# Optimization experiments

Hardware: AMD Instinct MI355X
Metric: run time of the kernel (lower is better)

Reference implementation:

```python
import jax, jax.numpy as jnp
import numpy as np

S = 14       # grid size
B = 2        # boxes per cell
C = 20       # classes
N_EL = B * 5 + C   # 30
L_COORD = 5.0
L_NOOBJ = 0.5
BATCH = 4096
NBOX = 16


def setup_inputs() -> dict:
    key = jax.random.key(0)
    k1, k2, k3, k4 = jax.random.split(key, 4)
    prediction = jax.random.uniform(k1, (BATCH, S * S * N_EL), dtype=jnp.float32)
    # well-formed ground-truth boxes: centers in (0.05,0.95), sizes in (0.02,0.3)
    cxcy = jax.random.uniform(k2, (BATCH, NBOX, 2), minval=0.05, maxval=0.95, dtype=jnp.float32)
    wh = jax.random.uniform(k3, (BATCH, NBOX, 2), minval=0.02, maxval=0.3, dtype=jnp.float32)
    boxes = jnp.concatenate([cxcy - wh / 2, cxcy + wh / 2], axis=-1)  # x1,y1,x2,y2
    classes = jax.random.randint(k4, (BATCH, NBOX), 0, C, dtype=jnp.int32)
    return {"prediction": prediction, "boxes": boxes, "classes": classes}


def _encode(boxes, classes):
    """Vectorized version of YoloLoss.encode: scatter boxes into SxS grid cells.
    Faithful detail: class one-hot goes to channel 9+class (the original's
    off-by-one: class 0 lands on the 2nd confidence channel)."""
    bsz, nbox = classes.shape
    cell = 1.0 / S
    xy1, xy2 = boxes[..., :2], boxes[..., 2:]
    wh = xy2 - xy1
    cxcy = (xy1 + xy2) / 2
    ij = jnp.clip(jnp.ceil(cxcy / cell) - 1, 0, S - 1)          # [b,nbox,2] (x,y)
    dxy = cxcy / cell - ij                                      # delta inside cell
    ij = ij.astype(jnp.int32)
    one = jnp.ones_like(wh[..., :1])
    zcls = jnp.zeros(classes.shape + (C,), dtype=boxes.dtype)
    # layout: [dxy, wh, conf, dxy, wh, conf, class one-hots]
    base = jnp.concatenate([dxy, wh, one, dxy, wh, one, zcls], axis=-1)  # [b,nbox,30]
    cls_oh = jax.nn.one_hot(classes + (B * 5 - 1), N_EL, dtype=boxes.dtype)  # index 9+class
    vec = jnp.maximum(base, cls_oh)
    flat_idx = (jnp.arange(bsz, dtype=jnp.int32)[:, None] * (S * S)
                + ij[..., 1] * S + ij[..., 0]).reshape(-1)      # row-major (y,x)
    target = jnp.zeros((bsz * S * S, N_EL), dtype=boxes.dtype)
    return target.at[flat_idx].set(vec.reshape(-1, N_EL))


def _pairwise_iou(a, b):
    """a,b: [N,B,4] -> iou [N,B(pred),B(target)] (corner-format jaccard, as in
    the original, applied to (dx,dy,w,h) rows verbatim)."""
    a4 = a[:, :, None, :]
    b4 = b[:, None, :, :]
    lt = jnp.maximum(a4[..., :2], b4[..., :2])
    rb = jnp.minimum(a4[..., 2:], b4[..., 2:])
    whi = jnp.clip(rb - lt, 0.0)
    inter = whi[..., 0] * whi[..., 1]
    area_a = (a4[..., 2] - a4[..., 0]) * (a4[..., 3] - a4[..., 1])
    area_b = (b4[..., 2] - b4[..., 0]) * (b4[..., 3] - b4[..., 1])
    union = area_a + area_b - inter
    return inter / jnp.where(union == 0, 1.0, union)


def reference(prediction, boxes, classes):
    target = _encode(boxes, classes)                       # [bsz*S*S, 30]
    pred = prediction.reshape(-1, N_EL)
    coord = target[:, 4] > 0                               # cells containing objects
    coordf = coord.astype(pred.dtype)
    noobjf = (target[:, 4] == 0).astype(pred.dtype)

    conf_idx = jnp.array([4, 9])
    noobj_loss = jnp.sum(noobjf[:, None] * (pred[:, conf_idx] - target[:, conf_idx]) ** 2)
    class_loss = jnp.sum(coordf[:, None] * (pred[:, B * 5:] - target[:, B * 5:]) ** 2)

    bp = pred[:, :B * 5].reshape(-1, B, 5)                 # [N,B,5]
    bt = target[:, :B * 5].reshape(-1, B, 5)

    iou = _pairwise_iou(bp[..., :4], bt[..., :4])          # [N,B,B]
    max_index = jnp.argmax(iou, axis=1)                    # best pred per target box
    response = (max_index[:, None, :] == jnp.arange(B)[None, :, None]).any(-1)  # [N,B]
    resp = response & coord[:, None]
    respf = resp.astype(pred.dtype)

    contain_loss = jnp.sum(respf * (bp[..., 4] - bt[..., 4]) ** 2)
    bt_wh = jnp.where(resp[..., None], bt[..., 2:4], 1.0)  # guard sqrt at masked cells
    loc_loss = jnp.sum(respf * (((bp[..., :2] - bt[..., :2]) ** 2).sum(-1)
                                + ((jnp.sqrt(bp[..., 2:4]) - jnp.sqrt(bt_wh)) ** 2).sum(-1)))

    return L_COORD * loc_loss + contain_loss + L_NOOBJ * noobj_loss + class_loss
```

## Files before the change

### kernel.cpp

```cpp
#include <hip/hip_runtime.h>


#define SGRID 14
#define CELLS 196
#define NEL 30
#define NBOX 16
#define PRED_PER_BATCH 5880
#define STREAM_ITERS 12
#define STREAM_TPB 256
#define STREAM_CHUNK (STREAM_ITERS * STREAM_TPB)

__device__ __forceinline__ void block_reduce_store(float v, float* slot) {
    #pragma unroll
    for (int off = 32; off > 0; off >>= 1)
        v += __shfl_down(v, off, 64);
    __shared__ float w4[4];
    int tid = threadIdx.x;
    if ((tid & 63) == 0) w4[tid >> 6] = v;
    __syncthreads();
    if (tid == 0) *slot = w4[0] + w4[1] + w4[2] + w4[3];
}

__global__ __launch_bounds__(256) void encode_kernel(
    const float4* __restrict__ boxes, const int* __restrict__ classes,
    int* __restrict__ winner, int nbb)
{
    int t = blockIdx.x * 256 + threadIdx.x;
    if (t >= nbb) return;
    int b = t >> 4, k = t & 15;
    float4 bx = boxes[t];
    const float cellw = (float)(1.0 / 14.0);
    float cx = (bx.x + bx.z) * 0.5f, cy = (bx.y + bx.w) * 0.5f;
    float fx = cx / cellw, fy = cy / cellw;
    float fi = fminf(fmaxf(ceilf(fx) - 1.0f, 0.0f), 13.0f);
    float fj = fminf(fmaxf(ceilf(fy) - 1.0f, 0.0f), 13.0f);
    int cell = (int)fj * SGRID + (int)fi;
    int hot = 9 + classes[t];
    atomicMax(&winner[b * CELLS + cell], (k << 8) | hot);
}

__global__ __launch_bounds__(256) void stream_kernel(
    const float4* __restrict__ pred4, const int* __restrict__ winner,
    float* __restrict__ partials, int nvec)
{
    int base = blockIdx.x * STREAM_CHUNK + threadIdx.x;
    float loss = 0.0f;
    #pragma unroll
    for (int i = 0; i < STREAM_ITERS; ++i) {
        int e = base + i * STREAM_TPB;
        if (e < nvec) {
            float4 v = pred4[e];
            int g = e * 4;
            int cell = (int)((unsigned)g / 30u);
            int c0 = g - cell * 30;
            int m0 = winner[cell];
            int m1 = winner[cell + 1];
            float pv[4] = {v.x, v.y, v.z, v.w};
            #pragma unroll
            for (int j = 0; j < 4; ++j) {
                int cj = c0 + j;
                int cc = (cj >= 30) ? cj - 30 : cj;
                int m  = (cj >= 30) ? m1 : m0;
                bool isconf = (cc == 4) | (cc == 9);
                float wgt = isconf ? ((m < 0) ? 0.5f : 0.0f)
                                   : ((cc >= 10) ? ((m >= 0) ? 1.0f : 0.0f) : 0.0f);
                float tt = (cc == (m & 0xFF)) ? 1.0f : 0.0f;
                float d = pv[j] - tt;
                loss += wgt * d * d;
            }
        }
    }
    block_reduce_store(loss, &partials[blockIdx.x]);
}

__global__ __launch_bounds__(256) void obj_kernel(
    const float* __restrict__ pred, const float4* __restrict__ boxes,
    const int* __restrict__ winner, float* __restrict__ partials, int nbb)
{
    int t = blockIdx.x * 256 + threadIdx.x;
    float loss = 0.0f;
    if (t < nbb) {
        int b = t >> 4, k = t & 15;
        float4 bx = boxes[t];
        const float cellw = (float)(1.0 / 14.0);
        float w = bx.z - bx.x, h = bx.w - bx.y;
        float cx = (bx.x + bx.z) * 0.5f, cy = (bx.y + bx.w) * 0.5f;
        float fx = cx / cellw, fy = cy / cellw;
        float fi = fminf(fmaxf(ceilf(fx) - 1.0f, 0.0f), 13.0f);
        float fj = fminf(fmaxf(ceilf(fy) - 1.0f, 0.0f), 13.0f);
        float dx = fx - fi, dy = fy - fj;
        int idx = b * CELLS + (int)fj * SGRID + (int)fi;
        int wv = winner[idx];
        if ((wv >> 8) == k) {
            const float* p = pred + (size_t)idx * NEL;
            float a[10];
            #pragma unroll
            for (int j = 0; j < 5; ++j) {
                float2 v = *(const float2*)(p + 2 * j);
                a[2 * j] = v.x;  a[2 * j + 1] = v.y;
            }
            float area_t = (w - dx) * (h - dy);
            float iou[2];
            #pragma unroll
            for (int i = 0; i < 2; ++i) {
                const float* q = a + i * 5;
                float ltx = fmaxf(q[0], dx), lty = fmaxf(q[1], dy);
                float rbx = fminf(q[2], w),  rby = fminf(q[3], h);
                float wi = fmaxf(rbx - ltx, 0.0f);
                float hi = fmaxf(rby - lty, 0.0f);
                float inter  = wi * hi;
                float area_a = (q[2] - q[0]) * (q[3] - q[1]);
                float uni    = area_a + area_t - inter;
                iou[i] = inter / ((uni == 0.0f) ? 1.0f : uni);
            }
            int r = (iou[1] > iou[0]) ? 1 : 0;
            const float* q = a + r * 5;
            float dc = q[4] - 1.0f;
            loss += dc * dc;
            float lx = q[0] - dx, ly = q[1] - dy;
            float lw = sqrtf(q[2]) - sqrtf(w);
            float lh = sqrtf(q[3]) - sqrtf(h);
            loss += 5.0f * (lx * lx + ly * ly + lw * lw + lh * lh);
        }
    }
    block_reduce_store(loss, &partials[blockIdx.x]);
}

__global__ __launch_bounds__(256) void final_reduce_kernel(
    const float* __restrict__ partials, float* __restrict__ out, int n)
{
    float s = 0.0f;
    for (int i = threadIdx.x; i < n; i += 256) s += partials[i];
    #pragma unroll
    for (int off = 32; off > 0; off >>= 1)
        s += __shfl_down(s, off, 64);
    __shared__ float w4[4];
    if ((threadIdx.x & 63) == 0) w4[threadIdx.x >> 6] = s;
    __syncthreads();
    if (threadIdx.x == 0) out[0] = w4[0] + w4[1] + w4[2] + w4[3];
}

extern "C" void kernel_launch(void* const* d_in, const int* in_sizes, int n_in,
                              void* d_out, int out_size, void* d_ws, size_t ws_size,
                              hipStream_t stream) {
    const float* pred    = (const float*)d_in[0];
    const float* boxes   = (const float*)d_in[1];
    const int*   classes = (const int*)d_in[2];
    float* out = (float*)d_out;

    const int batch = in_sizes[0] / PRED_PER_BATCH;
    const int total = batch * CELLS;
    const int nbb   = batch * NBOX;
    const int nvec  = total * NEL / 4;

    const int sblocks = (nvec + STREAM_CHUNK - 1) / STREAM_CHUNK;
    const int oblocks = (nbb + 255) / 256;
    const int nparts  = sblocks + oblocks;

    int*   winner   = (int*)d_ws;
    float* partials = (float*)((char*)d_ws + (size_t)(total + 1) * sizeof(int));

    hipMemsetAsync(winner, 0xFF, (size_t)(total + 1) * sizeof(int), stream);
    encode_kernel<<<dim3((nbb + 255) / 256), dim3(256), 0, stream>>>(
        (const float4*)boxes, classes, winner, nbb);
    stream_kernel<<<dim3(sblocks), dim3(256), 0, stream>>>(
        (const float4*)pred, winner, partials, nvec);
    obj_kernel<<<dim3(oblocks), dim3(256), 0, stream>>>(
        pred, (const float4*)boxes, winner, partials + sblocks, nbb);
    final_reduce_kernel<<<dim3(1), dim3(256), 0, stream>>>(partials, out, nparts);
}
```

Baseline: 159.4 us.

## Fuse encode, stream and object-loss kernels into one block-local kernel

Merges the memset, encode, streaming loss and object loss kernels into a single kernel. Each block builds the cell-winner table for the rows it covers in shared memory using shared atomics, then streams its chunk of predictions and handles the object-cell loss for rows that start inside its chunk. This removes three launches, the global winner array, and its memset and global atomics. In exchange, each block recomputes winners for up to four rows from the boxes, and the extra sync and setup work lands before the streaming loop.

```diff
diff --git a/kernel.cpp b/kernel.cpp
--- a/kernel.cpp
+++ b/kernel.cpp
@@ -6,61 +6,69 @@
 #define NEL 30
 #define NBOX 16
 #define PRED_PER_BATCH 5880
+#define VEC_PER_ROW 1470
 #define STREAM_ITERS 12
 #define STREAM_TPB 256
 #define STREAM_CHUNK (STREAM_ITERS * STREAM_TPB)
+#define WIN_TILE (4 * CELLS + 4)
 
-__device__ __forceinline__ void block_reduce_store(float v, float* slot) {
+__global__ __launch_bounds__(256) void yolo_fused_kernel(
+    const float4* __restrict__ pred4,
+    const float4* __restrict__ boxes,
+    const int*    __restrict__ classes,
+    float* __restrict__ partials,
+    int nvec, int nrows)
+{
+    __shared__ int   s_win[WIN_TILE];
+    __shared__ float s_w4[4];
+
+    const int tid = threadIdx.x;
+    const int v0  = blockIdx.x * STREAM_CHUNK;
+    const int r0  = v0 / VEC_PER_ROW;
+    const float cellw = (float)(1.0 / 14.0);
+
     #pragma unroll
-    for (int off = 32; off > 0; off >>= 1)
-        v += __shfl_down(v, off, 64);
-    __shared__ float w4[4];
-    int tid = threadIdx.x;
-    if ((tid & 63) == 0) w4[tid >> 6] = v;
+    for (int i = 0; i < (WIN_TILE + STREAM_TPB - 1) / STREAM_TPB; ++i) {
+        int idx = tid + i * STREAM_TPB;
+        if (idx < WIN_TILE) s_win[idx] = -1;
+    }
     __syncthreads();
-    if (tid == 0) *slot = w4[0] + w4[1] + w4[2] + w4[3];
-}
+    if (tid < 4 * NBOX) {
+        int rr = tid >> 4, row = r0 + rr, k = tid & 15;
+        if (row < nrows) {
+            float4 bx = boxes[row * NBOX + k];
+            float cx = (bx.x + bx.z) * 0.5f, cy = (bx.y + bx.w) * 0.5f;
+            float fx = cx / cellw, fy = cy / cellw;
+            float fi = fminf(fmaxf(ceilf(fx) - 1.0f, 0.0f), 13.0f);
+            float fj = fminf(fmaxf(ceilf(fy) - 1.0f, 0.0f), 13.0f);
+            int cell = (int)fj * SGRID + (int)fi;
+            int hot  = 9 + classes[row * NBOX + k];
+            atomicMax(&s_win[rr * CELLS + cell], (k << 8) | hot);
+        }
+    }
+    __syncthreads();
 
-__global__ __launch_bounds__(256) void encode_kernel(
-    const float4* __restrict__ boxes, const int* __restrict__ classes,
-    int* __restrict__ winner, int nbb)
-{
-    int t = blockIdx.x * 256 + threadIdx.x;
-    if (t >= nbb) return;
-    int b = t >> 4, k = t & 15;
-    float4 bx = boxes[t];
-    const float cellw = (float)(1.0 / 14.0);
-    float cx = (bx.x + bx.z) * 0.5f, cy = (bx.y + bx.w) * 0.5f;
-    float fx = cx / cellw, fy = cy / cellw;
-    float fi = fminf(fmaxf(ceilf(fx) - 1.0f, 0.0f), 13.0f);
-    float fj = fminf(fmaxf(ceilf(fy) - 1.0f, 0.0f), 13.0f);
-    int cell = (int)fj * SGRID + (int)fi;
-    int hot = 9 + classes[t];
-    atomicMax(&winner[b * CELLS + cell], (k << 8) | hot);
-}
-
-__global__ __launch_bounds__(256) void stream_kernel(
-    const float4* __restrict__ pred4, const int* __restrict__ winner,
-    float* __restrict__ partials, int nvec)
-{
-    int base = blockIdx.x * STREAM_CHUNK + threadIdx.x;
+    const int cellbase = r0 * CELLS;
     float loss = 0.0f;
+    const bool full = (v0 + STREAM_CHUNK) <= nvec;
     #pragma unroll
     for (int i = 0; i < STREAM_ITERS; ++i) {
-        int e = base + i * STREAM_TPB;
-        if (e < nvec) {
+        int e = v0 + tid + i * STREAM_TPB;
+        if (full || e < nvec) {
             float4 v = pred4[e];
-            int g = e * 4;
+            int g    = e * 4;
             int cell = (int)((unsigned)g / 30u);
-            int c0 = g - cell * 30;
-            int m0 = winner[cell];
-            int m1 = winner[cell + 1];
+            int c0   = g - cell * 30;
+            int lc   = cell - cellbase;
+            int m0 = s_win[lc];
+            int m1 = s_win[lc + 1];
             float pv[4] = {v.x, v.y, v.z, v.w};
             #pragma unroll
             for (int j = 0; j < 4; ++j) {
                 int cj = c0 + j;
-                int cc = (cj >= 30) ? cj - 30 : cj;
-                int m  = (cj >= 30) ? m1 : m0;
+                bool str = cj >= 30;
+                int cc = str ? cj - 30 : cj;
+                int m  = str ? m1 : m0;
                 bool isconf = (cc == 4) | (cc == 9);
                 float wgt = isconf ? ((m < 0) ? 0.5f : 0.0f)
                                    : ((cc >= 10) ? ((m >= 0) ? 1.0f : 0.0f) : 0.0f);
@@ -70,60 +78,61 @@
             }
         }
     }
-    block_reduce_store(loss, &partials[blockIdx.x]);
-}
 
-__global__ __launch_bounds__(256) void obj_kernel(
-    const float* __restrict__ pred, const float4* __restrict__ boxes,
-    const int* __restrict__ winner, float* __restrict__ partials, int nbb)
-{
-    int t = blockIdx.x * 256 + threadIdx.x;
-    float loss = 0.0f;
-    if (t < nbb) {
-        int b = t >> 4, k = t & 15;
-        float4 bx = boxes[t];
-        const float cellw = (float)(1.0 / 14.0);
-        float w = bx.z - bx.x, h = bx.w - bx.y;
-        float cx = (bx.x + bx.z) * 0.5f, cy = (bx.y + bx.w) * 0.5f;
-        float fx = cx / cellw, fy = cy / cellw;
-        float fi = fminf(fmaxf(ceilf(fx) - 1.0f, 0.0f), 13.0f);
-        float fj = fminf(fmaxf(ceilf(fy) - 1.0f, 0.0f), 13.0f);
-        float dx = fx - fi, dy = fy - fj;
-        int idx = b * CELLS + (int)fj * SGRID + (int)fi;
-        int wv = winner[idx];
-        if ((wv >> 8) == k) {
-            const float* p = pred + (size_t)idx * NEL;
-            float a[10];
-            #pragma unroll
-            for (int j = 0; j < 5; ++j) {
-                float2 v = *(const float2*)(p + 2 * j);
-                a[2 * j] = v.x;  a[2 * j + 1] = v.y;
+    if (tid < 4 * NBOX) {
+        int rr = tid >> 4, row = r0 + rr, k = tid & 15;
+        int rstart = row * VEC_PER_ROW;
+        if (row < nrows && rstart >= v0 && rstart < v0 + STREAM_CHUNK) {
+            float4 bx = boxes[row * NBOX + k];
+            float w = bx.z - bx.x, h = bx.w - bx.y;
+            float cx = (bx.x + bx.z) * 0.5f, cy = (bx.y + bx.w) * 0.5f;
+            float fx = cx / cellw, fy = cy / cellw;
+            float fi = fminf(fmaxf(ceilf(fx) - 1.0f, 0.0f), 13.0f);
+            float fj = fminf(fmaxf(ceilf(fy) - 1.0f, 0.0f), 13.0f);
+            float dx = fx - fi, dy = fy - fj;
+            int cell = (int)fj * SGRID + (int)fi;
+            int wv = s_win[rr * CELLS + cell];
+            if ((wv >> 8) == k) {
+                const float* p = (const float*)pred4 + (size_t)(row * CELLS + cell) * NEL;
+                float a[10];
+                #pragma unroll
+                for (int j = 0; j < 5; ++j) {
+                    float2 v = *(const float2*)(p + 2 * j);
+                    a[2 * j] = v.x;  a[2 * j + 1] = v.y;
+                }
+                float area_t = (w - dx) * (h - dy);
+                float iou[2];
+                #pragma unroll
+                for (int i = 0; i < 2; ++i) {
+                    const float* q = a + i * 5;
+                    float ltx = fmaxf(q[0], dx), lty = fmaxf(q[1], dy);
+                    float rbx = fminf(q[2], w),  rby = fminf(q[3], h);
+                    float wi = fmaxf(rbx - ltx, 0.0f);
+                    float hi = fmaxf(rby - lty, 0.0f);
+                    float inter  = wi * hi;
+                    float area_a = (q[2] - q[0]) * (q[3] - q[1]);
+                    float uni    = area_a + area_t - inter;
+                    iou[i] = inter / ((uni == 0.0f) ? 1.0f : uni);
+                }
+                int r = (iou[1] > iou[0]) ? 1 : 0;
+                const float* q = a + r * 5;
+                float dc = q[4] - 1.0f;
+                loss += dc * dc;
+                float lx = q[0] - dx, ly = q[1] - dy;
+                float lw = sqrtf(q[2]) - sqrtf(w);
+                float lh = sqrtf(q[3]) - sqrtf(h);
+                loss += 5.0f * (lx * lx + ly * ly + lw * lw + lh * lh);
             }
-            float area_t = (w - dx) * (h - dy);
-            float iou[2];
-            #pragma unroll
-            for (int i = 0; i < 2; ++i) {
-                const float* q = a + i * 5;
-                float ltx = fmaxf(q[0], dx), lty = fmaxf(q[1], dy);
-                float rbx = fminf(q[2], w),  rby = fminf(q[3], h);
-                float wi = fmaxf(rbx - ltx, 0.0f);
-                float hi = fmaxf(rby - lty, 0.0f);
-                float inter  = wi * hi;
-                float area_a = (q[2] - q[0]) * (q[3] - q[1]);
-                float uni    = area_a + area_t - inter;
-                iou[i] = inter / ((uni == 0.0f) ? 1.0f : uni);
-            }
-            int r = (iou[1] > iou[0]) ? 1 : 0;
-            const float* q = a + r * 5;
-            float dc = q[4] - 1.0f;
-            loss += dc * dc;
-            float lx = q[0] - dx, ly = q[1] - dy;
-            float lw = sqrtf(q[2]) - sqrtf(w);
-            float lh = sqrtf(q[3]) - sqrtf(h);
-            loss += 5.0f * (lx * lx + ly * ly + lw * lw + lh * lh);
         }
     }
-    block_reduce_store(loss, &partials[blockIdx.x]);
+
+    #pragma unroll
+    for (int off = 32; off > 0; off >>= 1)
+        loss += __shfl_down(loss, off, 64);
+    if ((tid & 63) == 0) s_w4[tid >> 6] = loss;
+    __syncthreads();
+    if (tid == 0)
+        partials[blockIdx.x] = s_w4[0] + s_w4[1] + s_w4[2] + s_w4[3];
 }
 
 __global__ __launch_bounds__(256) void final_reduce_kernel(
@@ -148,24 +157,13 @@
     const int*   classes = (const int*)d_in[2];
     float* out = (float*)d_out;
 
-    const int batch = in_sizes[0] / PRED_PER_BATCH;
-    const int total = batch * CELLS;
-    const int nbb   = batch * NBOX;
-    const int nvec  = total * NEL / 4;
+    const int nrows = in_sizes[0] / PRED_PER_BATCH;
+    const int nvec  = nrows * PRED_PER_BATCH / 4;
+    const int sblocks = (nvec + STREAM_CHUNK - 1) / STREAM_CHUNK;
 
-    const int sblocks = (nvec + STREAM_CHUNK - 1) / STREAM_CHUNK;
-    const int oblocks = (nbb + 255) / 256;
-    const int nparts  = sblocks + oblocks;
+    float* partials = (float*)d_ws;
 
-    int*   winner   = (int*)d_ws;
-    float* partials = (float*)((char*)d_ws + (size_t)(total + 1) * sizeof(int));
-
-    hipMemsetAsync(winner, 0xFF, (size_t)(total + 1) * sizeof(int), stream);
-    encode_kernel<<<dim3((nbb + 255) / 256), dim3(256), 0, stream>>>(
-        (const float4*)boxes, classes, winner, nbb);
-    stream_kernel<<<dim3(sblocks), dim3(256), 0, stream>>>(
-        (const float4*)pred, winner, partials, nvec);
-    obj_kernel<<<dim3(oblocks), dim3(256), 0, stream>>>(
-        pred, (const float4*)boxes, winner, partials + sblocks, nbb);
-    final_reduce_kernel<<<dim3(1), dim3(256), 0, stream>>>(partials, out, nparts);
+    yolo_fused_kernel<<<dim3(sblocks), dim3(STREAM_TPB), 0, stream>>>(
+        (const float4*)pred, (const float4*)boxes, classes, partials, nvec, nrows);
+    final_reduce_kernel<<<dim3(1), dim3(256), 0, stream>>>(partials, out, sblocks);
 }
```

After: 146.8 us. 7.9% less time.
